# Performance work log

Measured on AMD Instinct MI355X. Metric: run time of the kernel, lower is better.

The kernel has to match this reference:

```python
import jax, jax.numpy as jnp
from jax import lax
import numpy as np

P = 32      # num_series
H = 128     # hidden units
B = 32      # batch
T = 256     # sequence length

def setup_inputs() -> dict:
    key = jax.random.key(0)
    ks = jax.random.split(key, 8)
    s = 1.0 / np.sqrt(H)
    X     = jax.random.normal(ks[0], (B, T, P), dtype=jnp.float32)
    # per-network LSTM weights, PyTorch gate order (i, f, g, o) stacked in 4H
    W_ih  = jax.random.uniform(ks[1], (P, 4 * H, P), dtype=jnp.float32, minval=-s, maxval=s)
    W_hh  = jax.random.uniform(ks[2], (P, 4 * H, H), dtype=jnp.float32, minval=-s, maxval=s)
    b_ih  = jax.random.uniform(ks[3], (P, 4 * H), dtype=jnp.float32, minval=-s, maxval=s)
    b_hh  = jax.random.uniform(ks[4], (P, 4 * H), dtype=jnp.float32, minval=-s, maxval=s)
    # Conv1d(hidden, 1, kernel_size=1) == per-timestep linear H -> 1, per network
    W_out = jax.random.uniform(ks[5], (P, H), dtype=jnp.float32, minval=-s, maxval=s)
    b_out = jax.random.uniform(ks[6], (P,), dtype=jnp.float32, minval=-s, maxval=s)
    return {"X": X, "W_ih": W_ih, "W_hh": W_hh, "b_ih": b_ih,
            "b_hh": b_hh, "W_out": W_out, "b_out": b_out}

def reference(X, W_ih, W_hh, b_ih, b_hh, W_out, b_out):
    # X: (B, T, P); p independent 1-layer LSTMs run on the same input,
    # batched along a network axis n (size P) with distinct weights.
    # Precompute input projections for all steps/networks: (T, B, P, 4H)
    xproj = jnp.einsum('btd,nkd->tbnk', X, W_ih) + b_ih + b_hh

    def step(carry, xp_t):
        h, c = carry                                   # (B, P, H) each
        gates = xp_t + jnp.einsum('bnh,nkh->bnk', h, W_hh)
        i, f, g, o = jnp.split(gates, 4, axis=-1)
        i = jax.nn.sigmoid(i)
        f = jax.nn.sigmoid(f)
        g = jnp.tanh(g)
        o = jax.nn.sigmoid(o)
        c = f * c + i * g
        h = o * jnp.tanh(c)
        return (h, c), h

    h0 = jnp.zeros((X.shape[0], W_ih.shape[0], W_hh.shape[2]), X.dtype)
    (_, _), hs = lax.scan(step, (h0, h0), xproj)        # hs: (T, B, P, H)
    # 1x1 conv head per network, then concat over networks -> (B, T, P)
    pred = jnp.einsum('tbnh,nh->btn', hs, W_out) + b_out
    return pred
```

## Files before the change

kernel.cpp:

```cpp
#include <hip/hip_runtime.h>
#include <stdint.h>

#define NP 32
#define NH 128
#define NB 32
#define NT 256
#define FH 512

typedef __attribute__((ext_vector_type(4))) float float4_t;
typedef __attribute__((ext_vector_type(8))) __bf16 bf16x8;
typedef __attribute__((ext_vector_type(4))) __bf16 bf16x4;

static __device__ __forceinline__ float4_t mfma_bf16(bf16x8 a, bf16x8 b, float4_t c) {
  return __builtin_amdgcn_mfma_f32_16x16x32_bf16(a, b, c, 0, 0, 0);
}

#define LOG2E 1.4426950408889634f

#define BAR() __asm__ volatile("s_waitcnt lgkmcnt(0)\n\ts_barrier" ::: "memory")


__global__ __launch_bounds__(512, 1) void xcvt(
    const float* __restrict__ X, __bf16* __restrict__ Xb)
{
  const int i = (blockIdx.x * 512 + threadIdx.x) * 4;
  float4_t v = *(const float4_t*)(X + i);
  bf16x4 o;
#pragma unroll
  for (int j = 0; j < 4; ++j) o[j] = (__bf16)v[j];
  *(bf16x4*)(Xb + i) = o;
}

__global__ __attribute__((amdgpu_flat_work_group_size(512, 512),
                          amdgpu_waves_per_eu(2, 2)))
void clstm_fused3(
    const __bf16* __restrict__ Xb, const float* __restrict__ Wih,
    const float* __restrict__ Whh, const float* __restrict__ bih,
    const float* __restrict__ bhh, const float* __restrict__ Wout,
    const float* __restrict__ bout, float* __restrict__ out)
{
  const int net = blockIdx.x >> 3, bq = blockIdx.x & 7;
  const int tid = threadIdx.x;
  const int w = tid >> 6, lane = tid & 63;
  const int quad = lane >> 4, l16 = lane & 15;

  __shared__ __bf16 hfrag[2][4][4][4][8];

  { ((int*)hfrag)[tid] = 0; }
  __syncthreads();

  bf16x8 bfrag[4][5];
  float4_t bias4[4];
#pragma unroll
  for (int g = 0; g < 4; ++g) {
    const float scale = (g == 2) ? (-2.0f*LOG2E) : (-LOG2E);
    const int col = g*NH + w*16 + l16;
#pragma unroll
    for (int kc = 0; kc < 5; ++kc) {
      const float* src = (kc == 0) ? (Wih + ((size_t)net*FH + col)*NP + quad*8)
                                   : (Whh + ((size_t)net*FH + col)*NH + (kc-1)*32 + quad*8);
      bf16x8 bf;
#pragma unroll
      for (int j = 0; j < 8; ++j) bf[j] = (__bf16)(src[j] * scale);
      bfrag[g][kc] = bf;
    }
    const float b = (bih[net*FH + col] + bhh[net*FH + col]) * scale;
    bias4[g] = (float4_t){b, b, b, b};
  }

  bf16x8 wof[4];
#pragma unroll
  for (int kc = 0; kc < 4; ++kc) {
    const float* wp = Wout + net*NH + kc*32 + quad*8;
#pragma unroll
    for (int j = 0; j < 8; ++j) wof[kc][j] = (__bf16)wp[j];
  }
  const float bo = bout[net];

  float cs = 0.f;
  const float S2 = -2.0f*LOG2E;

  int xoff = (bq*4 + (l16 & 3))*(NT*NP) + quad*8;

  const int kcp = w >> 1, q2 = ((w & 1) << 1) | (l16 >> 3), jj = l16 & 7;

  float* outp = out + ((size_t)bq*4)*(NT*NP) + net;

  bf16x8 ax = *(const bf16x8*)(Xb + xoff);
  xoff += NP;

  for (int t = 0; t < NT; ++t) {
    const int rd = t & 1, wr = rd ^ 1;

    bf16x8 ah[4];
#pragma unroll
    for (int kc = 0; kc < 4; ++kc)
      ah[kc] = *(const bf16x8*)&hfrag[rd][kc][quad][l16 & 3][0];

    float4_t acc[4];
#pragma unroll
    for (int g = 0; g < 4; ++g)
      acc[g] = mfma_bf16(ax, bfrag[g][0], bias4[g]);

    if (t + 1 < NT)
      ax = *(const bf16x8*)(Xb + xoff);
    xoff += NP;

#pragma unroll
    for (int kc = 0; kc < 4; ++kc)
#pragma unroll
      for (int g = 0; g < 4; ++g)
        acc[g] = mfma_bf16(ah[kc], bfrag[g][kc+1], acc[g]);

    float gv[4];
#pragma unroll
    for (int g = 0; g < 4; ++g) {
      float a01 = (quad & 1) ? acc[g][1] : acc[g][0];
      float a23 = (quad & 1) ? acc[g][3] : acc[g][2];
      gv[g] = (quad & 2) ? a23 : a01;
    }

    float h;
    {
      float ei = __builtin_amdgcn_exp2f(gv[0]);
      float ig = __builtin_amdgcn_rcpf(1.0f + ei);
      float ef = __builtin_amdgcn_exp2f(gv[1]);
      float fg = __builtin_amdgcn_rcpf(1.0f + ef);
      float eg = __builtin_amdgcn_exp2f(fminf(gv[2], 126.0f));
      float rg = __builtin_amdgcn_rcpf(1.0f + eg);
      float t0 = S2 * rg;
      float gg2 = t0 - t0 * eg;
      float eo = __builtin_amdgcn_exp2f(gv[3]);
      float og = __builtin_amdgcn_rcpf(1.0f + eo);
      cs = fg * cs + ig * gg2;
      float ec = __builtin_amdgcn_exp2f(fminf(cs, 126.0f));
      float rc = __builtin_amdgcn_rcpf(1.0f + ec);
      float th = rc - ec * rc;
      h = og * th;
    }

    hfrag[wr][kcp][q2][quad][jj] = (__bf16)h;

    if (w == 0 && t > 0) {
      float4_t p0 = {bo, bo, bo, bo};
      float4_t p1 = {0.f, 0.f, 0.f, 0.f};
      p0 = mfma_bf16(ah[0], wof[0], p0);
      p1 = mfma_bf16(ah[2], wof[2], p1);
      p0 = mfma_bf16(ah[1], wof[1], p0);
      p1 = mfma_bf16(ah[3], wof[3], p1);
      float4_t po = p0 + p1;
      if (lane == 0) {
#pragma unroll
        for (int r = 0; r < 4; ++r)
          outp[(size_t)r*(NT*NP) + (t - 1)*NP] = po[r];
      }
    }

    BAR();
  }

  if (w == 0) {
    bf16x8 ahf[4];
#pragma unroll
    for (int kc = 0; kc < 4; ++kc)
      ahf[kc] = *(const bf16x8*)&hfrag[NT & 1][kc][quad][l16 & 3][0];
    float4_t p0 = {bo, bo, bo, bo};
    float4_t p1 = {0.f, 0.f, 0.f, 0.f};
    p0 = mfma_bf16(ahf[0], wof[0], p0);
    p1 = mfma_bf16(ahf[2], wof[2], p1);
    p0 = mfma_bf16(ahf[1], wof[1], p0);
    p1 = mfma_bf16(ahf[3], wof[3], p1);
    float4_t po = p0 + p1;
    if (lane == 0) {
#pragma unroll
      for (int r = 0; r < 4; ++r)
        outp[(size_t)r*(NT*NP) + (NT - 1)*NP] = po[r];
    }
  }
}

__global__ __launch_bounds__(512, 1) void clstm_fused_fb(
    const float* __restrict__ X, const float* __restrict__ Wih,
    const float* __restrict__ Whh, const float* __restrict__ bih,
    const float* __restrict__ bhh, const float* __restrict__ Wout,
    const float* __restrict__ bout, float* __restrict__ out)
{
  const int net = blockIdx.x >> 3, bq = blockIdx.x & 7;
  const int tid = threadIdx.x;
  const int w = tid >> 6, lane = tid & 63;
  const int quad = lane >> 4, l16 = lane & 15;

  __shared__ __bf16 hfrag[2][4][4][4][8];
  { ((int*)hfrag)[tid] = 0; }
  __syncthreads();

  bf16x8 bfrag[4][5];
  float4_t bias4[4];
#pragma unroll
  for (int g = 0; g < 4; ++g) {
    const float scale = (g == 2) ? (-2.0f*LOG2E) : (-LOG2E);
    const int col = g*NH + w*16 + l16;
#pragma unroll
    for (int kc = 0; kc < 5; ++kc) {
      const float* src = (kc == 0) ? (Wih + ((size_t)net*FH + col)*NP + quad*8)
                                   : (Whh + ((size_t)net*FH + col)*NH + (kc-1)*32 + quad*8);
      bf16x8 bf;
#pragma unroll
      for (int j = 0; j < 8; ++j) bf[j] = (__bf16)(src[j] * scale);
      bfrag[g][kc] = bf;
    }
    const float b = (bih[net*FH + col] + bhh[net*FH + col]) * scale;
    bias4[g] = (float4_t){b, b, b, b};
  }

  bf16x8 wof[4];
#pragma unroll
  for (int kc = 0; kc < 4; ++kc) {
    const float* wp = Wout + net*NH + kc*32 + quad*8;
#pragma unroll
    for (int j = 0; j < 8; ++j) wof[kc][j] = (__bf16)wp[j];
  }
  const float bo = bout[net];

  float cs = 0.f;
  const float S2 = -2.0f*LOG2E;

  const float* xrow = X + (size_t)(bq*4 + (l16 & 3))*(NT*NP) + quad*8;
  const int kcp = w >> 1, q2 = ((w & 1) << 1) | (l16 >> 3), jj = l16 & 7;
  float* outp = out + ((size_t)bq*4)*(NT*NP) + net;

  bf16x8 ax;
  {
    float xv0[8];
    *(float4_t*)&xv0[0] = *(const float4_t*)xrow;
    *(float4_t*)&xv0[4] = *(const float4_t*)(xrow + 4);
#pragma unroll
    for (int j = 0; j < 8; ++j) ax[j] = (__bf16)xv0[j];
  }
  const float* xp = xrow + NP;
  float xv[8] = {0.f,0.f,0.f,0.f,0.f,0.f,0.f,0.f};

  for (int t = 0; t < NT; ++t) {
    const int rd = t & 1, wr = rd ^ 1;
    bf16x8 ah[4];
#pragma unroll
    for (int kc = 0; kc < 4; ++kc)
      ah[kc] = *(const bf16x8*)&hfrag[rd][kc][quad][l16 & 3][0];
    float4_t accx[4];
#pragma unroll
    for (int g = 0; g < 4; ++g)
      accx[g] = mfma_bf16(ax, bfrag[g][0], bias4[g]);
    if (t + 1 < NT) {
      *(float4_t*)&xv[0] = *(const float4_t*)xp;
      *(float4_t*)&xv[4] = *(const float4_t*)(xp + 4);
    }
    float4_t acc[4];
#pragma unroll
    for (int g = 0; g < 4; ++g) {
      float4_t a0 = mfma_bf16(ah[0], bfrag[g][1], accx[g]);
      float4_t a1 = mfma_bf16(ah[2], bfrag[g][3], (float4_t){0.f,0.f,0.f,0.f});
      a0 = mfma_bf16(ah[1], bfrag[g][2], a0);
      a1 = mfma_bf16(ah[3], bfrag[g][4], a1);
      acc[g] = a0 + a1;
    }
    float gv[4];
#pragma unroll
    for (int g = 0; g < 4; ++g) {
      float a01 = (quad & 1) ? acc[g][1] : acc[g][0];
      float a23 = (quad & 1) ? acc[g][3] : acc[g][2];
      gv[g] = (quad & 2) ? a23 : a01;
    }
    float h;
    {
      float ei = __builtin_amdgcn_exp2f(gv[0]);
      float ig = __builtin_amdgcn_rcpf(1.0f + ei);
      float ef = __builtin_amdgcn_exp2f(gv[1]);
      float fg = __builtin_amdgcn_rcpf(1.0f + ef);
      float eg = __builtin_amdgcn_exp2f(fminf(gv[2], 126.0f));
      float rg = __builtin_amdgcn_rcpf(1.0f + eg);
      float t0 = S2 * rg;
      float gg2 = t0 - t0 * eg;
      float eo = __builtin_amdgcn_exp2f(gv[3]);
      float og = __builtin_amdgcn_rcpf(1.0f + eo);
      cs = fg * cs + ig * gg2;
      float ec = __builtin_amdgcn_exp2f(fminf(cs, 126.0f));
      float rc = __builtin_amdgcn_rcpf(1.0f + ec);
      float th = rc - ec * rc;
      h = og * th;
    }
    hfrag[wr][kcp][q2][quad][jj] = (__bf16)h;
    if (w == 0 && t > 0) {
      float4_t p0 = {bo, bo, bo, bo};
      float4_t p1 = {0.f, 0.f, 0.f, 0.f};
      p0 = mfma_bf16(ah[0], wof[0], p0);
      p1 = mfma_bf16(ah[2], wof[2], p1);
      p0 = mfma_bf16(ah[1], wof[1], p0);
      p1 = mfma_bf16(ah[3], wof[3], p1);
      float4_t po = p0 + p1;
      if (lane == 0) {
#pragma unroll
        for (int r = 0; r < 4; ++r)
          outp[(size_t)r*(NT*NP) + (t - 1)*NP] = po[r];
      }
    }
#pragma unroll
    for (int j = 0; j < 8; ++j) ax[j] = (__bf16)xv[j];
    xp += NP;
    BAR();
  }

  if (w == 0) {
    bf16x8 ahf[4];
#pragma unroll
    for (int kc = 0; kc < 4; ++kc)
      ahf[kc] = *(const bf16x8*)&hfrag[NT & 1][kc][quad][l16 & 3][0];
    float4_t p0 = {bo, bo, bo, bo};
    float4_t p1 = {0.f, 0.f, 0.f, 0.f};
    p0 = mfma_bf16(ahf[0], wof[0], p0);
    p1 = mfma_bf16(ahf[2], wof[2], p1);
    p0 = mfma_bf16(ahf[1], wof[1], p0);
    p1 = mfma_bf16(ahf[3], wof[3], p1);
    float4_t po = p0 + p1;
    if (lane == 0) {
#pragma unroll
      for (int r = 0; r < 4; ++r)
        outp[(size_t)r*(NT*NP) + (NT - 1)*NP] = po[r];
    }
  }
}

extern "C" void kernel_launch(void* const* d_in, const int* in_sizes, int n_in,
                              void* d_out, int out_size, void* d_ws, size_t ws_size,
                              hipStream_t stream) {
  const float* X    = (const float*)d_in[0];
  const float* Wih  = (const float*)d_in[1];
  const float* Whh  = (const float*)d_in[2];
  const float* bih  = (const float*)d_in[3];
  const float* bhh  = (const float*)d_in[4];
  const float* Wout = (const float*)d_in[5];
  const float* bout = (const float*)d_in[6];
  float* out = (float*)d_out;
  (void)in_sizes; (void)n_in; (void)out_size;

  const size_t need = (size_t)NB*NT*NP*2;
  if (d_ws != nullptr && ws_size >= need) {
    __bf16* wsX = (__bf16*)d_ws;
    xcvt<<<128, 512, 0, stream>>>(X, wsX);
    clstm_fused3<<<256, 512, 0, stream>>>(wsX, Wih, Whh, bih, bhh, Wout,
                                          bout, out);
  } else {
    clstm_fused_fb<<<256, 512, 0, stream>>>(X, Wih, Whh, bih, bhh, Wout,
                                            bout, out);
  }
}
```

Baseline: 216.7 us.

## Interleave gate MFMAs with sigmoid math and rotate output head across waves

The recurrent step is split into two MFMA halves: the input and forget gates are computed first and their exp/rcp math runs, pinned by sched_barriers, while the cell and output gate MFMAs are issued. The time loop is unrolled by two so the ping-pong LDS buffer indices become compile-time constants. The 1x1 output-head MFMAs rotate across waves by timestep instead of always running on wave 0, which spreads that extra work evenly. The sched_barriers fix the instruction order and can stop the compiler from finding a better interleave.

After: 220.3 us. No clear change (+1.7%).

```diff
diff --git a/kernel.cpp b/kernel.cpp
--- a/kernel.cpp
+++ b/kernel.cpp
@@ -18,6 +18,7 @@
 #define LOG2E 1.4426950408889634f
 
 #define BAR() __asm__ volatile("s_waitcnt lgkmcnt(0)\n\ts_barrier" ::: "memory")
+#define SB()  __builtin_amdgcn_sched_barrier(0)
 
 
 __global__ __launch_bounds__(512, 1) void xcvt(
@@ -33,7 +34,7 @@
 
 __global__ __attribute__((amdgpu_flat_work_group_size(512, 512),
                           amdgpu_waves_per_eu(2, 2)))
-void clstm_fused3(
+void clstm_fused4(
     const __bf16* __restrict__ Xb, const float* __restrict__ Wih,
     const float* __restrict__ Whh, const float* __restrict__ bih,
     const float* __restrict__ bhh, const float* __restrict__ Wout,
@@ -89,29 +90,191 @@
   bf16x8 ax = *(const bf16x8*)(Xb + xoff);
   xoff += NP;
 
+#define STEP(RD, WR, T_)                                                      \
+  do {                                                                        \
+       \
+    bf16x8 ah0 = *(const bf16x8*)&hfrag[RD][0][quad][l16 & 3][0];             \
+    bf16x8 ah1 = *(const bf16x8*)&hfrag[RD][1][quad][l16 & 3][0];             \
+    bf16x8 ah2 = *(const bf16x8*)&hfrag[RD][2][quad][l16 & 3][0];             \
+    bf16x8 ah3 = *(const bf16x8*)&hfrag[RD][3][quad][l16 & 3][0];             \
+    float4_t a0 = mfma_bf16(ax, bfrag[0][0], bias4[0]);                       \
+    float4_t a1 = mfma_bf16(ax, bfrag[1][0], bias4[1]);                       \
+    float4_t a2 = mfma_bf16(ax, bfrag[2][0], bias4[2]);                       \
+    float4_t a3 = mfma_bf16(ax, bfrag[3][0], bias4[3]);                       \
+    if ((T_) + 1 < NT) ax = *(const bf16x8*)(Xb + xoff);                      \
+    xoff += NP;                                                               \
+    a0 = mfma_bf16(ah0, bfrag[0][1], a0);                                     \
+    a1 = mfma_bf16(ah0, bfrag[1][1], a1);                                     \
+    a0 = mfma_bf16(ah1, bfrag[0][2], a0);                                     \
+    a1 = mfma_bf16(ah1, bfrag[1][2], a1);                                     \
+    a0 = mfma_bf16(ah2, bfrag[0][3], a0);                                     \
+    a1 = mfma_bf16(ah2, bfrag[1][3], a1);                                     \
+    a0 = mfma_bf16(ah3, bfrag[0][4], a0);                                     \
+    a1 = mfma_bf16(ah3, bfrag[1][4], a1);                                     \
+    SB();                                                                     \
+          \
+    float gi = (quad & 2) ? ((quad & 1) ? a0[3] : a0[2])                      \
+                          : ((quad & 1) ? a0[1] : a0[0]);                     \
+    float gf = (quad & 2) ? ((quad & 1) ? a1[3] : a1[2])                      \
+                          : ((quad & 1) ? a1[1] : a1[0]);                     \
+    float ei = __builtin_amdgcn_exp2f(gi);                                    \
+    float ig = __builtin_amdgcn_rcpf(1.0f + ei);                              \
+    float ef = __builtin_amdgcn_exp2f(gf);                                    \
+    float fg = __builtin_amdgcn_rcpf(1.0f + ef);                              \
+    SB();                                                                     \
+                                                     \
+    a2 = mfma_bf16(ah0, bfrag[2][1], a2);                                     \
+    a3 = mfma_bf16(ah0, bfrag[3][1], a3);                                     \
+    a2 = mfma_bf16(ah1, bfrag[2][2], a2);                                     \
+    a3 = mfma_bf16(ah1, bfrag[3][2], a3);                                     \
+    a2 = mfma_bf16(ah2, bfrag[2][3], a2);                                     \
+    a3 = mfma_bf16(ah2, bfrag[3][3], a3);                                     \
+    a2 = mfma_bf16(ah3, bfrag[2][4], a2);                                     \
+    a3 = mfma_bf16(ah3, bfrag[3][4], a3);                                     \
+    SB();                                                                     \
+                          \
+    float gg = (quad & 2) ? ((quad & 1) ? a2[3] : a2[2])                      \
+                          : ((quad & 1) ? a2[1] : a2[0]);                     \
+    float go = (quad & 2) ? ((quad & 1) ? a3[3] : a3[2])                      \
+                          : ((quad & 1) ? a3[1] : a3[0]);                     \
+    float eg = __builtin_amdgcn_exp2f(fminf(gg, 126.0f));                     \
+    float rg = __builtin_amdgcn_rcpf(1.0f + eg);                              \
+    float t0 = S2 * rg;                                                       \
+    float gg2 = t0 - t0 * eg;                                 \
+    float eo = __builtin_amdgcn_exp2f(go);                                    \
+    float og = __builtin_amdgcn_rcpf(1.0f + eo);                              \
+    cs = fg * cs + ig * gg2;                                      \
+    float ec = __builtin_amdgcn_exp2f(fminf(cs, 126.0f));                     \
+    float rc = __builtin_amdgcn_rcpf(1.0f + ec);                              \
+    float h_ = og * (rc - ec * rc);                          \
+    hfrag[WR][kcp][q2][quad][jj] = (__bf16)h_;                                \
+    if ((T_) > 0 && w == ((T_) & 7)) {                                        \
+      float4_t p0 = {bo, bo, bo, bo};                                         \
+      float4_t p1 = {0.f, 0.f, 0.f, 0.f};                                     \
+      p0 = mfma_bf16(ah0, wof[0], p0);                                        \
+      p1 = mfma_bf16(ah2, wof[2], p1);                                        \
+      p0 = mfma_bf16(ah1, wof[1], p0);                                        \
+      p1 = mfma_bf16(ah3, wof[3], p1);                                        \
+      float4_t po = p0 + p1;                                                  \
+      if (lane == 0) {                                                        \
+        _Pragma("unroll")                                                     \
+        for (int r = 0; r < 4; ++r)                                           \
+          outp[(size_t)r*(NT*NP) + ((T_) - 1)*NP] = po[r];                    \
+      }                                                                       \
+    }                                                                         \
+    BAR();                                                                    \
+  } while (0)
+
+  for (int t = 0; t < NT; t += 2) {
+    STEP(0, 1, t);
+    STEP(1, 0, t + 1);
+  }
+#undef STEP
+
+  if (w == 0) {
+    bf16x8 ahf[4];
+#pragma unroll
+    for (int kc = 0; kc < 4; ++kc)
+      ahf[kc] = *(const bf16x8*)&hfrag[NT & 1][kc][quad][l16 & 3][0];
+    float4_t p0 = {bo, bo, bo, bo};
+    float4_t p1 = {0.f, 0.f, 0.f, 0.f};
+    p0 = mfma_bf16(ahf[0], wof[0], p0);
+    p1 = mfma_bf16(ahf[2], wof[2], p1);
+    p0 = mfma_bf16(ahf[1], wof[1], p0);
+    p1 = mfma_bf16(ahf[3], wof[3], p1);
+    float4_t po = p0 + p1;
+    if (lane == 0) {
+#pragma unroll
+      for (int r = 0; r < 4; ++r)
+        outp[(size_t)r*(NT*NP) + (NT - 1)*NP] = po[r];
+    }
+  }
+}
+
+__global__ __launch_bounds__(512, 1) void clstm_fused_fb(
+    const float* __restrict__ X, const float* __restrict__ Wih,
+    const float* __restrict__ Whh, const float* __restrict__ bih,
+    const float* __restrict__ bhh, const float* __restrict__ Wout,
+    const float* __restrict__ bout, float* __restrict__ out)
+{
+  const int net = blockIdx.x >> 3, bq = blockIdx.x & 7;
+  const int tid = threadIdx.x;
+  const int w = tid >> 6, lane = tid & 63;
+  const int quad = lane >> 4, l16 = lane & 15;
+
+  __shared__ __bf16 hfrag[2][4][4][4][8];
+  { ((int*)hfrag)[tid] = 0; }
+  __syncthreads();
+
+  bf16x8 bfrag[4][5];
+  float4_t bias4[4];
+#pragma unroll
+  for (int g = 0; g < 4; ++g) {
+    const float scale = (g == 2) ? (-2.0f*LOG2E) : (-LOG2E);
+    const int col = g*NH + w*16 + l16;
+#pragma unroll
+    for (int kc = 0; kc < 5; ++kc) {
+      const float* src = (kc == 0) ? (Wih + ((size_t)net*FH + col)*NP + quad*8)
+                                   : (Whh + ((size_t)net*FH + col)*NH + (kc-1)*32 + quad*8);
+      bf16x8 bf;
+#pragma unroll
+      for (int j = 0; j < 8; ++j) bf[j] = (__bf16)(src[j] * scale);
+      bfrag[g][kc] = bf;
+    }
+    const float b = (bih[net*FH + col] + bhh[net*FH + col]) * scale;
+    bias4[g] = (float4_t){b, b, b, b};
+  }
+
+  bf16x8 wof[4];
+#pragma unroll
+  for (int kc = 0; kc < 4; ++kc) {
+    const float* wp = Wout + net*NH + kc*32 + quad*8;
+#pragma unroll
+    for (int j = 0; j < 8; ++j) wof[kc][j] = (__bf16)wp[j];
+  }
+  const float bo = bout[net];
+
+  float cs = 0.f;
+  const float S2 = -2.0f*LOG2E;
+
+  const float* xrow = X + (size_t)(bq*4 + (l16 & 3))*(NT*NP) + quad*8;
+  const int kcp = w >> 1, q2 = ((w & 1) << 1) | (l16 >> 3), jj = l16 & 7;
+  float* outp = out + ((size_t)bq*4)*(NT*NP) + net;
+
+  bf16x8 ax;
+  {
+    float xv0[8];
+    *(float4_t*)&xv0[0] = *(const float4_t*)xrow;
+    *(float4_t*)&xv0[4] = *(const float4_t*)(xrow + 4);
+#pragma unroll
+    for (int j = 0; j < 8; ++j) ax[j] = (__bf16)xv0[j];
+  }
+  const float* xp = xrow + NP;
+  float xv[8] = {0.f,0.f,0.f,0.f,0.f,0.f,0.f,0.f};
+
   for (int t = 0; t < NT; ++t) {
     const int rd = t & 1, wr = rd ^ 1;
-
     bf16x8 ah[4];
 #pragma unroll
     for (int kc = 0; kc < 4; ++kc)
       ah[kc] = *(const bf16x8*)&hfrag[rd][kc][quad][l16 & 3][0];
-
+    float4_t accx[4];
+#pragma unroll
+    for (int g = 0; g < 4; ++g)
+      accx[g] = mfma_bf16(ax, bfrag[g][0], bias4[g]);
+    if (t + 1 < NT) {
+      *(float4_t*)&xv[0] = *(const float4_t*)xp;
+      *(float4_t*)&xv[4] = *(const float4_t*)(xp + 4);
+    }
     float4_t acc[4];
 #pragma unroll
-    for (int g = 0; g < 4; ++g)
-      acc[g] = mfma_bf16(ax, bfrag[g][0], bias4[g]);
-
-    if (t + 1 < NT)
-      ax = *(const bf16x8*)(Xb + xoff);
-    xoff += NP;
-
-#pragma unroll
-    for (int kc = 0; kc < 4; ++kc)
-#pragma unroll
-      for (int g = 0; g < 4; ++g)
-        acc[g] = mfma_bf16(ah[kc], bfrag[g][kc+1], acc[g]);
-
+    for (int g = 0; g < 4; ++g) {
+      float4_t a0 = mfma_bf16(ah[0], bfrag[g][1], accx[g]);
+      float4_t a1 = mfma_bf16(ah[2], bfrag[g][3], (float4_t){0.f,0.f,0.f,0.f});
+      a0 = mfma_bf16(ah[1], bfrag[g][2], a0);
+      a1 = mfma_bf16(ah[3], bfrag[g][4], a1);
+      acc[g] = a0 + a1;
+    }
     float gv[4];
 #pragma unroll
     for (int g = 0; g < 4; ++g) {
@@ -119,7 +282,6 @@
       float a23 = (quad & 1) ? acc[g][3] : acc[g][2];
       gv[g] = (quad & 2) ? a23 : a01;
     }
-
     float h;
     {
       float ei = __builtin_amdgcn_exp2f(gv[0]);
@@ -138,156 +300,6 @@
       float th = rc - ec * rc;
       h = og * th;
     }
-
-    hfrag[wr][kcp][q2][quad][jj] = (__bf16)h;
-
-    if (w == 0 && t > 0) {
-      float4_t p0 = {bo, bo, bo, bo};
-      float4_t p1 = {0.f, 0.f, 0.f, 0.f};
-      p0 = mfma_bf16(ah[0], wof[0], p0);
-      p1 = mfma_bf16(ah[2], wof[2], p1);
-      p0 = mfma_bf16(ah[1], wof[1], p0);
-      p1 = mfma_bf16(ah[3], wof[3], p1);
-      float4_t po = p0 + p1;
-      if (lane == 0) {
-#pragma unroll
-        for (int r = 0; r < 4; ++r)
-          outp[(size_t)r*(NT*NP) + (t - 1)*NP] = po[r];
-      }
-    }
-
-    BAR();
-  }
-
-  if (w == 0) {
-    bf16x8 ahf[4];
-#pragma unroll
-    for (int kc = 0; kc < 4; ++kc)
-      ahf[kc] = *(const bf16x8*)&hfrag[NT & 1][kc][quad][l16 & 3][0];
-    float4_t p0 = {bo, bo, bo, bo};
-    float4_t p1 = {0.f, 0.f, 0.f, 0.f};
-    p0 = mfma_bf16(ahf[0], wof[0], p0);
-    p1 = mfma_bf16(ahf[2], wof[2], p1);
-    p0 = mfma_bf16(ahf[1], wof[1], p0);
-    p1 = mfma_bf16(ahf[3], wof[3], p1);
-    float4_t po = p0 + p1;
-    if (lane == 0) {
-#pragma unroll
-      for (int r = 0; r < 4; ++r)
-        outp[(size_t)r*(NT*NP) + (NT - 1)*NP] = po[r];
-    }
-  }
-}
-
-__global__ __launch_bounds__(512, 1) void clstm_fused_fb(
-    const float* __restrict__ X, const float* __restrict__ Wih,
-    const float* __restrict__ Whh, const float* __restrict__ bih,
-    const float* __restrict__ bhh, const float* __restrict__ Wout,
-    const float* __restrict__ bout, float* __restrict__ out)
-{
-  const int net = blockIdx.x >> 3, bq = blockIdx.x & 7;
-  const int tid = threadIdx.x;
-  const int w = tid >> 6, lane = tid & 63;
-  const int quad = lane >> 4, l16 = lane & 15;
-
-  __shared__ __bf16 hfrag[2][4][4][4][8];
-  { ((int*)hfrag)[tid] = 0; }
-  __syncthreads();
-
-  bf16x8 bfrag[4][5];
-  float4_t bias4[4];
-#pragma unroll
-  for (int g = 0; g < 4; ++g) {
-    const float scale = (g == 2) ? (-2.0f*LOG2E) : (-LOG2E);
-    const int col = g*NH + w*16 + l16;
-#pragma unroll
-    for (int kc = 0; kc < 5; ++kc) {
-      const float* src = (kc == 0) ? (Wih + ((size_t)net*FH + col)*NP + quad*8)
-                                   : (Whh + ((size_t)net*FH + col)*NH + (kc-1)*32 + quad*8);
-      bf16x8 bf;
-#pragma unroll
-      for (int j = 0; j < 8; ++j) bf[j] = (__bf16)(src[j] * scale);
-      bfrag[g][kc] = bf;
-    }
-    const float b = (bih[net*FH + col] + bhh[net*FH + col]) * scale;
-    bias4[g] = (float4_t){b, b, b, b};
-  }
-
-  bf16x8 wof[4];
-#pragma unroll
-  for (int kc = 0; kc < 4; ++kc) {
-    const float* wp = Wout + net*NH + kc*32 + quad*8;
-#pragma unroll
-    for (int j = 0; j < 8; ++j) wof[kc][j] = (__bf16)wp[j];
-  }
-  const float bo = bout[net];
-
-  float cs = 0.f;
-  const float S2 = -2.0f*LOG2E;
-
-  const float* xrow = X + (size_t)(bq*4 + (l16 & 3))*(NT*NP) + quad*8;
-  const int kcp = w >> 1, q2 = ((w & 1) << 1) | (l16 >> 3), jj = l16 & 7;
-  float* outp = out + ((size_t)bq*4)*(NT*NP) + net;
-
-  bf16x8 ax;
-  {
-    float xv0[8];
-    *(float4_t*)&xv0[0] = *(const float4_t*)xrow;
-    *(float4_t*)&xv0[4] = *(const float4_t*)(xrow + 4);
-#pragma unroll
-    for (int j = 0; j < 8; ++j) ax[j] = (__bf16)xv0[j];
-  }
-  const float* xp = xrow + NP;
-  float xv[8] = {0.f,0.f,0.f,0.f,0.f,0.f,0.f,0.f};
-
-  for (int t = 0; t < NT; ++t) {
-    const int rd = t & 1, wr = rd ^ 1;
-    bf16x8 ah[4];
-#pragma unroll
-    for (int kc = 0; kc < 4; ++kc)
-      ah[kc] = *(const bf16x8*)&hfrag[rd][kc][quad][l16 & 3][0];
-    float4_t accx[4];
-#pragma unroll
-    for (int g = 0; g < 4; ++g)
-      accx[g] = mfma_bf16(ax, bfrag[g][0], bias4[g]);
-    if (t + 1 < NT) {
-      *(float4_t*)&xv[0] = *(const float4_t*)xp;
-      *(float4_t*)&xv[4] = *(const float4_t*)(xp + 4);
-    }
-    float4_t acc[4];
-#pragma unroll
-    for (int g = 0; g < 4; ++g) {
-      float4_t a0 = mfma_bf16(ah[0], bfrag[g][1], accx[g]);
-      float4_t a1 = mfma_bf16(ah[2], bfrag[g][3], (float4_t){0.f,0.f,0.f,0.f});
-      a0 = mfma_bf16(ah[1], bfrag[g][2], a0);
-      a1 = mfma_bf16(ah[3], bfrag[g][4], a1);
-      acc[g] = a0 + a1;
-    }
-    float gv[4];
-#pragma unroll
-    for (int g = 0; g < 4; ++g) {
-      float a01 = (quad & 1) ? acc[g][1] : acc[g][0];
-      float a23 = (quad & 1) ? acc[g][3] : acc[g][2];
-      gv[g] = (quad & 2) ? a23 : a01;
-    }
-    float h;
-    {
-      float ei = __builtin_amdgcn_exp2f(gv[0]);
-      float ig = __builtin_amdgcn_rcpf(1.0f + ei);
-      float ef = __builtin_amdgcn_exp2f(gv[1]);
-      float fg = __builtin_amdgcn_rcpf(1.0f + ef);
-      float eg = __builtin_amdgcn_exp2f(fminf(gv[2], 126.0f));
-      float rg = __builtin_amdgcn_rcpf(1.0f + eg);
-      float t0 = S2 * rg;
-      float gg2 = t0 - t0 * eg;
-      float eo = __builtin_amdgcn_exp2f(gv[3]);
-      float og = __builtin_amdgcn_rcpf(1.0f + eo);
-      cs = fg * cs + ig * gg2;
-      float ec = __builtin_amdgcn_exp2f(fminf(cs, 126.0f));
-      float rc = __builtin_amdgcn_rcpf(1.0f + ec);
-      float th = rc - ec * rc;
-      h = og * th;
-    }
     hfrag[wr][kcp][q2][quad][jj] = (__bf16)h;
     if (w == 0 && t > 0) {
       float4_t p0 = {bo, bo, bo, bo};
@@ -346,7 +358,7 @@
   if (d_ws != nullptr && ws_size >= need) {
     __bf16* wsX = (__bf16*)d_ws;
     xcvt<<<128, 512, 0, stream>>>(X, wsX);
-    clstm_fused3<<<256, 512, 0, stream>>>(wsX, Wih, Whh, bih, bhh, Wout,
+    clstm_fused4<<<256, 512, 0, stream>>>(wsX, Wih, Whh, bih, bhh, Wout,
                                           bout, out);
   } else {
     clstm_fused_fb<<<256, 512, 0, stream>>>(X, Wih, Whh, bih, bhh, Wout,
```

## Interleave per-gate MFMA chains with activations and rotate output-head wave

Applied to the files above, without the earlier changes.

The main kernel is restructured so each gate's MFMA chain is followed directly by its activation, with sched_barriers between gates. Half the waves process the gates in a different order so that matrix and transcendental work from different waves overlap. The output-head projection now rotates across waves by timestep instead of always landing on wave 0, which spreads out that extra latency. The block index mapping also swaps net and batch-quarter, which changes which blocks share a CU or XCD.

Measured after the change: 234.2 us. +8.1%, slower.

```diff
diff --git a/kernel.cpp b/kernel.cpp
--- a/kernel.cpp
+++ b/kernel.cpp
@@ -18,6 +18,7 @@
 #define LOG2E 1.4426950408889634f
 
 #define BAR() __asm__ volatile("s_waitcnt lgkmcnt(0)\n\ts_barrier" ::: "memory")
+#define SB()  __builtin_amdgcn_sched_barrier(0)
 
 
 __global__ __launch_bounds__(512, 1) void xcvt(
@@ -33,8 +34,161 @@
 
 __global__ __attribute__((amdgpu_flat_work_group_size(512, 512),
                           amdgpu_waves_per_eu(2, 2)))
-void clstm_fused3(
+void clstm_fused5(
     const __bf16* __restrict__ Xb, const float* __restrict__ Wih,
+    const float* __restrict__ Whh, const float* __restrict__ bih,
+    const float* __restrict__ bhh, const float* __restrict__ Wout,
+    const float* __restrict__ bout, float* __restrict__ out)
+{
+  const int net = blockIdx.x & 31, bq = blockIdx.x >> 5;
+  const int tid = threadIdx.x;
+  const int w = tid >> 6, lane = tid & 63;
+  const int quad = lane >> 4, l16 = lane & 15;
+
+  __shared__ __bf16 hfrag[2][4][4][4][8];
+
+  { ((int*)hfrag)[tid] = 0; }
+  __syncthreads();
+
+  bf16x8 bfrag[4][5];
+  float4_t bias4[4];
+#pragma unroll
+  for (int g = 0; g < 4; ++g) {
+    const float scale = (g == 2) ? (-2.0f*LOG2E) : (-LOG2E);
+    const int col = g*NH + w*16 + l16;
+#pragma unroll
+    for (int kc = 0; kc < 5; ++kc) {
+      const float* src = (kc == 0) ? (Wih + ((size_t)net*FH + col)*NP + quad*8)
+                                   : (Whh + ((size_t)net*FH + col)*NH + (kc-1)*32 + quad*8);
+      bf16x8 bf;
+#pragma unroll
+      for (int j = 0; j < 8; ++j) bf[j] = (__bf16)(src[j] * scale);
+      bfrag[g][kc] = bf;
+    }
+    const float b = (bih[net*FH + col] + bhh[net*FH + col]) * scale;
+    bias4[g] = (float4_t){b, b, b, b};
+  }
+
+  bf16x8 wof[4];
+#pragma unroll
+  for (int kc = 0; kc < 4; ++kc) {
+    const float* wp = Wout + net*NH + kc*32 + quad*8;
+#pragma unroll
+    for (int j = 0; j < 8; ++j) wof[kc][j] = (__bf16)wp[j];
+  }
+  const float bo = bout[net];
+
+  float cs = 0.f;
+  const float S2 = -2.0f*LOG2E;
+
+  int xoff = (bq*4 + (l16 & 3))*(NT*NP) + quad*8;
+
+  const int kcp = w >> 1, q2 = ((w & 1) << 1) | (l16 >> 3), jj = l16 & 7;
+
+  float* outp = out + ((size_t)bq*4)*(NT*NP) + net;
+
+  bf16x8 ax = *(const bf16x8*)(Xb + xoff);
+  xoff += NP;
+
+#define CHAIN(G)                                                              \
+    a##G = mfma_bf16(ax,  bfrag[G][0], bias4[G]);                             \
+    a##G = mfma_bf16(ah0, bfrag[G][1], a##G);                                 \
+    a##G = mfma_bf16(ah1, bfrag[G][2], a##G);                                 \
+    a##G = mfma_bf16(ah2, bfrag[G][3], a##G);                                 \
+    a##G = mfma_bf16(ah3, bfrag[G][4], a##G);
+
+#define SEL(G) ((quad & 2) ? ((quad & 1) ? a##G[3] : a##G[2])                 \
+                           : ((quad & 1) ? a##G[1] : a##G[0]))
+
+#define ACT_I { float e = __builtin_amdgcn_exp2f(SEL(0));                     \
+                ig = __builtin_amdgcn_rcpf(1.0f + e); }
+#define ACT_F { float e = __builtin_amdgcn_exp2f(SEL(1));                     \
+                fg = __builtin_amdgcn_rcpf(1.0f + e); }
+#define ACT_G { float e = __builtin_amdgcn_exp2f(fminf(SEL(2), 126.0f));      \
+                float r = __builtin_amdgcn_rcpf(1.0f + e);                    \
+                float t0 = S2 * r; gg2 = t0 - t0 * e; }
+#define ACT_O { float e = __builtin_amdgcn_exp2f(SEL(3));                     \
+                og = __builtin_amdgcn_rcpf(1.0f + e); }
+
+  for (int t = 0; t < NT; ++t) {
+    const int rd = t & 1, wr = rd ^ 1;
+
+    bf16x8 ah0 = *(const bf16x8*)&hfrag[rd][0][quad][l16 & 3][0];
+    bf16x8 ah1 = *(const bf16x8*)&hfrag[rd][1][quad][l16 & 3][0];
+    bf16x8 ah2 = *(const bf16x8*)&hfrag[rd][2][quad][l16 & 3][0];
+    bf16x8 ah3 = *(const bf16x8*)&hfrag[rd][3][quad][l16 & 3][0];
+
+    float4_t a0, a1, a2, a3;
+    float ig, fg, gg2, og;
+
+    if (w & 4) {
+      CHAIN(2) ACT_G SB();
+      CHAIN(3) ACT_O SB();
+      CHAIN(0) ACT_I SB();
+      CHAIN(1) ACT_F
+    } else {
+      CHAIN(0) ACT_I SB();
+      CHAIN(1) ACT_F SB();
+      CHAIN(2) ACT_G SB();
+      CHAIN(3) ACT_O
+    }
+
+    if (t + 1 < NT)
+      ax = *(const bf16x8*)(Xb + xoff);
+    xoff += NP;
+
+    cs = fg * cs + ig * gg2;
+    float ec = __builtin_amdgcn_exp2f(fminf(cs, 126.0f));
+    float rc = __builtin_amdgcn_rcpf(1.0f + ec);
+    float h = og * (rc - ec * rc);
+    hfrag[wr][kcp][q2][quad][jj] = (__bf16)h;
+
+    if (t > 0 && w == (t & 7)) {
+      float4_t p0 = {bo, bo, bo, bo};
+      float4_t p1 = {0.f, 0.f, 0.f, 0.f};
+      p0 = mfma_bf16(ah0, wof[0], p0);
+      p1 = mfma_bf16(ah2, wof[2], p1);
+      p0 = mfma_bf16(ah1, wof[1], p0);
+      p1 = mfma_bf16(ah3, wof[3], p1);
+      float4_t po = p0 + p1;
+      if (lane == 0) {
+#pragma unroll
+        for (int r = 0; r < 4; ++r)
+          outp[(size_t)r*(NT*NP) + (t - 1)*NP] = po[r];
+      }
+    }
+
+    BAR();
+  }
+#undef CHAIN
+#undef SEL
+#undef ACT_I
+#undef ACT_F
+#undef ACT_G
+#undef ACT_O
+
+  if (w == 0) {
+    bf16x8 ahf[4];
+#pragma unroll
+    for (int kc = 0; kc < 4; ++kc)
+      ahf[kc] = *(const bf16x8*)&hfrag[NT & 1][kc][quad][l16 & 3][0];
+    float4_t p0 = {bo, bo, bo, bo};
+    float4_t p1 = {0.f, 0.f, 0.f, 0.f};
+    p0 = mfma_bf16(ahf[0], wof[0], p0);
+    p1 = mfma_bf16(ahf[2], wof[2], p1);
+    p0 = mfma_bf16(ahf[1], wof[1], p0);
+    p1 = mfma_bf16(ahf[3], wof[3], p1);
+    float4_t po = p0 + p1;
+    if (lane == 0) {
+#pragma unroll
+      for (int r = 0; r < 4; ++r)
+        outp[(size_t)r*(NT*NP) + (NT - 1)*NP] = po[r];
+    }
+  }
+}
+
+__global__ __launch_bounds__(512, 1) void clstm_fused_fb(
+    const float* __restrict__ X, const float* __restrict__ Wih,
     const float* __restrict__ Whh, const float* __restrict__ bih,
     const float* __restrict__ bhh, const float* __restrict__ Wout,
     const float* __restrict__ bout, float* __restrict__ out)
@@ -45,7 +199,6 @@
   const int quad = lane >> 4, l16 = lane & 15;
 
   __shared__ __bf16 hfrag[2][4][4][4][8];
-
   { ((int*)hfrag)[tid] = 0; }
   __syncthreads();
 
@@ -80,38 +233,44 @@
   float cs = 0.f;
   const float S2 = -2.0f*LOG2E;
 
-  int xoff = (bq*4 + (l16 & 3))*(NT*NP) + quad*8;
-
+  const float* xrow = X + (size_t)(bq*4 + (l16 & 3))*(NT*NP) + quad*8;
   const int kcp = w >> 1, q2 = ((w & 1) << 1) | (l16 >> 3), jj = l16 & 7;
-
   float* outp = out + ((size_t)bq*4)*(NT*NP) + net;
 
-  bf16x8 ax = *(const bf16x8*)(Xb + xoff);
-  xoff += NP;
+  bf16x8 ax;
+  {
+    float xv0[8];
+    *(float4_t*)&xv0[0] = *(const float4_t*)xrow;
+    *(float4_t*)&xv0[4] = *(const float4_t*)(xrow + 4);
+#pragma unroll
+    for (int j = 0; j < 8; ++j) ax[j] = (__bf16)xv0[j];
+  }
+  const float* xp = xrow + NP;
+  float xv[8] = {0.f,0.f,0.f,0.f,0.f,0.f,0.f,0.f};
 
   for (int t = 0; t < NT; ++t) {
     const int rd = t & 1, wr = rd ^ 1;
-
     bf16x8 ah[4];
 #pragma unroll
     for (int kc = 0; kc < 4; ++kc)
       ah[kc] = *(const bf16x8*)&hfrag[rd][kc][quad][l16 & 3][0];
-
+    float4_t accx[4];
+#pragma unroll
+    for (int g = 0; g < 4; ++g)
+      accx[g] = mfma_bf16(ax, bfrag[g][0], bias4[g]);
+    if (t + 1 < NT) {
+      *(float4_t*)&xv[0] = *(const float4_t*)xp;
+      *(float4_t*)&xv[4] = *(const float4_t*)(xp + 4);
+    }
     float4_t acc[4];
 #pragma unroll
-    for (int g = 0; g < 4; ++g)
-      acc[g] = mfma_bf16(ax, bfrag[g][0], bias4[g]);
-
-    if (t + 1 < NT)
-      ax = *(const bf16x8*)(Xb + xoff);
-    xoff += NP;
-
-#pragma unroll
-    for (int kc = 0; kc < 4; ++kc)
-#pragma unroll
-      for (int g = 0; g < 4; ++g)
-        acc[g] = mfma_bf16(ah[kc], bfrag[g][kc+1], acc[g]);
-
+    for (int g = 0; g < 4; ++g) {
+      float4_t a0 = mfma_bf16(ah[0], bfrag[g][1], accx[g]);
+      float4_t a1 = mfma_bf16(ah[2], bfrag[g][3], (float4_t){0.f,0.f,0.f,0.f});
+      a0 = mfma_bf16(ah[1], bfrag[g][2], a0);
+      a1 = mfma_bf16(ah[3], bfrag[g][4], a1);
+      acc[g] = a0 + a1;
+    }
     float gv[4];
 #pragma unroll
     for (int g = 0; g < 4; ++g) {
@@ -119,7 +278,6 @@
       float a23 = (quad & 1) ? acc[g][3] : acc[g][2];
       gv[g] = (quad & 2) ? a23 : a01;
     }
-
     float h;
     {
       float ei = __builtin_amdgcn_exp2f(gv[0]);
@@ -138,156 +296,6 @@
       float th = rc - ec * rc;
       h = og * th;
     }
-
-    hfrag[wr][kcp][q2][quad][jj] = (__bf16)h;
-
-    if (w == 0 && t > 0) {
-      float4_t p0 = {bo, bo, bo, bo};
-      float4_t p1 = {0.f, 0.f, 0.f, 0.f};
-      p0 = mfma_bf16(ah[0], wof[0], p0);
-      p1 = mfma_bf16(ah[2], wof[2], p1);
-      p0 = mfma_bf16(ah[1], wof[1], p0);
-      p1 = mfma_bf16(ah[3], wof[3], p1);
-      float4_t po = p0 + p1;
-      if (lane == 0) {
-#pragma unroll
-        for (int r = 0; r < 4; ++r)
-          outp[(size_t)r*(NT*NP) + (t - 1)*NP] = po[r];
-      }
-    }
-
-    BAR();
-  }
-
-  if (w == 0) {
-    bf16x8 ahf[4];
-#pragma unroll
-    for (int kc = 0; kc < 4; ++kc)
-      ahf[kc] = *(const bf16x8*)&hfrag[NT & 1][kc][quad][l16 & 3][0];
-    float4_t p0 = {bo, bo, bo, bo};
-    float4_t p1 = {0.f, 0.f, 0.f, 0.f};
-    p0 = mfma_bf16(ahf[0], wof[0], p0);
-    p1 = mfma_bf16(ahf[2], wof[2], p1);
-    p0 = mfma_bf16(ahf[1], wof[1], p0);
-    p1 = mfma_bf16(ahf[3], wof[3], p1);
-    float4_t po = p0 + p1;
-    if (lane == 0) {
-#pragma unroll
-      for (int r = 0; r < 4; ++r)
-        outp[(size_t)r*(NT*NP) + (NT - 1)*NP] = po[r];
-    }
-  }
-}
-
-__global__ __launch_bounds__(512, 1) void clstm_fused_fb(
-    const float* __restrict__ X, const float* __restrict__ Wih,
-    const float* __restrict__ Whh, const float* __restrict__ bih,
-    const float* __restrict__ bhh, const float* __restrict__ Wout,
-    const float* __restrict__ bout, float* __restrict__ out)
-{
-  const int net = blockIdx.x >> 3, bq = blockIdx.x & 7;
-  const int tid = threadIdx.x;
-  const int w = tid >> 6, lane = tid & 63;
-  const int quad = lane >> 4, l16 = lane & 15;
-
-  __shared__ __bf16 hfrag[2][4][4][4][8];
-  { ((int*)hfrag)[tid] = 0; }
-  __syncthreads();
-
-  bf16x8 bfrag[4][5];
-  float4_t bias4[4];
-#pragma unroll
-  for (int g = 0; g < 4; ++g) {
-    const float scale = (g == 2) ? (-2.0f*LOG2E) : (-LOG2E);
-    const int col = g*NH + w*16 + l16;
-#pragma unroll
-    for (int kc = 0; kc < 5; ++kc) {
-      const float* src = (kc == 0) ? (Wih + ((size_t)net*FH + col)*NP + quad*8)
-                                   : (Whh + ((size_t)net*FH + col)*NH + (kc-1)*32 + quad*8);
-      bf16x8 bf;
-#pragma unroll
-      for (int j = 0; j < 8; ++j) bf[j] = (__bf16)(src[j] * scale);
-      bfrag[g][kc] = bf;
-    }
-    const float b = (bih[net*FH + col] + bhh[net*FH + col]) * scale;
-    bias4[g] = (float4_t){b, b, b, b};
-  }
-
-  bf16x8 wof[4];
-#pragma unroll
-  for (int kc = 0; kc < 4; ++kc) {
-    const float* wp = Wout + net*NH + kc*32 + quad*8;
-#pragma unroll
-    for (int j = 0; j < 8; ++j) wof[kc][j] = (__bf16)wp[j];
-  }
-  const float bo = bout[net];
-
-  float cs = 0.f;
-  const float S2 = -2.0f*LOG2E;
-
-  const float* xrow = X + (size_t)(bq*4 + (l16 & 3))*(NT*NP) + quad*8;
-  const int kcp = w >> 1, q2 = ((w & 1) << 1) | (l16 >> 3), jj = l16 & 7;
-  float* outp = out + ((size_t)bq*4)*(NT*NP) + net;
-
-  bf16x8 ax;
-  {
-    float xv0[8];
-    *(float4_t*)&xv0[0] = *(const float4_t*)xrow;
-    *(float4_t*)&xv0[4] = *(const float4_t*)(xrow + 4);
-#pragma unroll
-    for (int j = 0; j < 8; ++j) ax[j] = (__bf16)xv0[j];
-  }
-  const float* xp = xrow + NP;
-  float xv[8] = {0.f,0.f,0.f,0.f,0.f,0.f,0.f,0.f};
-
-  for (int t = 0; t < NT; ++t) {
-    const int rd = t & 1, wr = rd ^ 1;
-    bf16x8 ah[4];
-#pragma unroll
-    for (int kc = 0; kc < 4; ++kc)
-      ah[kc] = *(const bf16x8*)&hfrag[rd][kc][quad][l16 & 3][0];
-    float4_t accx[4];
-#pragma unroll
-    for (int g = 0; g < 4; ++g)
-      accx[g] = mfma_bf16(ax, bfrag[g][0], bias4[g]);
-    if (t + 1 < NT) {
-      *(float4_t*)&xv[0] = *(const float4_t*)xp;
-      *(float4_t*)&xv[4] = *(const float4_t*)(xp + 4);
-    }
-    float4_t acc[4];
-#pragma unroll
-    for (int g = 0; g < 4; ++g) {
-      float4_t a0 = mfma_bf16(ah[0], bfrag[g][1], accx[g]);
-      float4_t a1 = mfma_bf16(ah[2], bfrag[g][3], (float4_t){0.f,0.f,0.f,0.f});
-      a0 = mfma_bf16(ah[1], bfrag[g][2], a0);
-      a1 = mfma_bf16(ah[3], bfrag[g][4], a1);
-      acc[g] = a0 + a1;
-    }
-    float gv[4];
-#pragma unroll
-    for (int g = 0; g < 4; ++g) {
-      float a01 = (quad & 1) ? acc[g][1] : acc[g][0];
-      float a23 = (quad & 1) ? acc[g][3] : acc[g][2];
-      gv[g] = (quad & 2) ? a23 : a01;
-    }
-    float h;
-    {
-      float ei = __builtin_amdgcn_exp2f(gv[0]);
-      float ig = __builtin_amdgcn_rcpf(1.0f + ei);
-      float ef = __builtin_amdgcn_exp2f(gv[1]);
-      float fg = __builtin_amdgcn_rcpf(1.0f + ef);
-      float eg = __builtin_amdgcn_exp2f(fminf(gv[2], 126.0f));
-      float rg = __builtin_amdgcn_rcpf(1.0f + eg);
-      float t0 = S2 * rg;
-      float gg2 = t0 - t0 * eg;
-      float eo = __builtin_amdgcn_exp2f(gv[3]);
-      float og = __builtin_amdgcn_rcpf(1.0f + eo);
-      cs = fg * cs + ig * gg2;
-      float ec = __builtin_amdgcn_exp2f(fminf(cs, 126.0f));
-      float rc = __builtin_amdgcn_rcpf(1.0f + ec);
-      float th = rc - ec * rc;
-      h = og * th;
-    }
     hfrag[wr][kcp][q2][quad][jj] = (__bf16)h;
     if (w == 0 && t > 0) {
       float4_t p0 = {bo, bo, bo, bo};
@@ -346,7 +354,7 @@
   if (d_ws != nullptr && ws_size >= need) {
     __bf16* wsX = (__bf16*)d_ws;
     xcvt<<<128, 512, 0, stream>>>(X, wsX);
-    clstm_fused3<<<256, 512, 0, stream>>>(wsX, Wih, Whh, bih, bhh, Wout,
+    clstm_fused5<<<256, 512, 0, stream>>>(wsX, Wih, Whh, bih, bhh, Wout,
                                           bout, out);
   } else {
     clstm_fused_fb<<<256, 512, 0, stream>>>(X, Wih, Whh, bih, bhh, Wout,
```
